# Performance work log

Hardware: AMD Instinct MI355X
Metric: run time of the kernel (lower is better)

The kernel has to match this reference:

```python
import jax, jax.numpy as jnp
import numpy as np

B, S, D = 4, 2048, 1024
H, HD = 16, 64
FF = 4096
EPS = 1e-5
NEG = -1000000.0


def setup_inputs() -> dict:
    key = jax.random.key(0)
    ks = jax.random.split(key, 12)
    sc = lambda n: 1.0 / np.sqrt(n)
    return {
        "x": jax.random.normal(ks[0], (B, S, D), jnp.float32),
        "valid_lens": jax.random.randint(ks[1], (B,), 1, S, jnp.int32),
        "Wq": jax.random.normal(ks[2], (D, H * HD), jnp.float32) * sc(D),
        "Wk": jax.random.normal(ks[3], (D, H * HD), jnp.float32) * sc(D),
        "Wv": jax.random.normal(ks[4], (D, H * HD), jnp.float32) * sc(D),
        "Wo": jax.random.normal(ks[5], (H * HD, D), jnp.float32) * sc(H * HD),
        "W1": jax.random.normal(ks[6], (D, FF), jnp.float32) * sc(D),
        "b1": jnp.zeros((FF,), jnp.float32),
        "W2": jax.random.normal(ks[7], (FF, D), jnp.float32) * sc(FF),
        "b2": jnp.zeros((D,), jnp.float32),
        "g1": jnp.ones((D,), jnp.float32),
        "beta1": jnp.zeros((D,), jnp.float32),
        "g2": jnp.ones((D,), jnp.float32),
        "beta2": jnp.zeros((D,), jnp.float32),
    }


def _layernorm(x, g, b):
    mu = jnp.mean(x, axis=-1, keepdims=True)
    var = jnp.var(x, axis=-1, keepdims=True)
    return (x - mu) * jax.lax.rsqrt(var + EPS) * g + b


def _encoder_block(x, valid_lens, Wq, Wk, Wv, Wo, W1, b1, W2, b2, g1, beta1, g2, beta2):
    # multi-head attention (vectorized over heads; masked softmax as in original)
    q = (x @ Wq).reshape(B, S, H, HD)
    k = (x @ Wk).reshape(B, S, H, HD)
    v = (x @ Wv).reshape(B, S, H, HD)
    scores = jnp.einsum("bqhd,bkhd->bhqk", q, k) / np.sqrt(HD)
    # mask: key positions >= valid_len[b] set to -1e6 (matches python-loop masking)
    col = jnp.arange(S)[None, None, None, :]           # [1,1,1,S]
    mask = col < valid_lens[:, None, None, None]       # [B,1,1,S]
    scores = jnp.where(mask, scores, NEG)
    w = jax.nn.softmax(scores, axis=-1)
    attn = jnp.einsum("bhqk,bkhd->bqhd", w, v).reshape(B, S, H * HD)
    attn_out = attn @ Wo
    res1 = _layernorm(attn_out + x, g1, beta1)
    ff = jax.nn.relu(res1 @ W1 + b1) @ W2 + b2
    return _layernorm(ff + res1, g2, beta2)


def reference(x, valid_lens, Wq, Wk, Wv, Wo, W1, b1, W2, b2, g1, beta1, g2, beta2):
    return _encoder_block(x, valid_lens, Wq, Wk, Wv, Wo, W1, b1, W2, b2, g1, beta1, g2, beta2)
```

## Files before the change

### kernel.cpp

```cpp
#include <hip/hip_runtime.h>
#include <hip/hip_bf16.h>
#include <stdint.h>

#define BB 4
#define SS 2048
#define DD 1024
#define HH 16
#define HD 64
#define FF 4096
#define MM (BB * SS)
#define BH (BB * HH)

typedef __bf16 bf16x8 __attribute__((ext_vector_type(8)));
typedef float f32x4 __attribute__((ext_vector_type(4)));

static __device__ __forceinline__ unsigned short f2bf(float f) {
  union { float f; unsigned u; } v; v.f = f;
  unsigned r = v.u + 0x7fffu + ((v.u >> 16) & 1u);
  return (unsigned short)(r >> 16);
}

static __device__ __forceinline__ unsigned packbf2(float a, float b) {
  __hip_bfloat162 h = __float22bfloat162_rn(float2{a, b});
  union { __hip_bfloat162 h; unsigned u; } cv; cv.h = h; return cv.u;
}

#define GLD_LDS16(SRC, DST)                                          \
  __builtin_amdgcn_global_load_lds(                                  \
      (const __attribute__((address_space(1))) void*)(SRC),          \
      (__attribute__((address_space(3))) void*)(DST), 16, 0, 0)

__global__ __launch_bounds__(256) void cast_bf16_k(const float* __restrict__ in,
                                                   unsigned short* __restrict__ out) {
  size_t i = ((size_t)blockIdx.x * 256 + threadIdx.x) * 4;
  float4 v = *(const float4*)(in + i);
  ushort4 u;
  u.x = f2bf(v.x); u.y = f2bf(v.y); u.z = f2bf(v.z); u.w = f2bf(v.w);
  *(ushort4*)(out + i) = u;
}

__global__ __launch_bounds__(256) void transpose_cast_k(const float* __restrict__ in,
                                                        unsigned short* __restrict__ out,
                                                        int K, int N) {
  __shared__ float tile[32][33];
  int n0 = blockIdx.x * 32, k0 = blockIdx.y * 32;
  int tx = threadIdx.x, ty = threadIdx.y;
#pragma unroll
  for (int i = 0; i < 32; i += 8)
    tile[ty + i][tx] = in[(size_t)(k0 + ty + i) * N + n0 + tx];
  __syncthreads();
#pragma unroll
  for (int i = 0; i < 32; i += 8)
    out[(size_t)(n0 + ty + i) * K + k0 + tx] = f2bf(tile[tx][ty + i]);
}

template <int EPI, int BN>
__global__ __launch_bounds__(512, 2) void gemm256(const unsigned short* __restrict__ A,
                                                  const unsigned short* __restrict__ BT,
                                                  const float* __restrict__ bias,
                                                  void* __restrict__ Cout,
                                                  int N, int K) {
  constexpr int BM = 256;
  constexpr int WN = BN / 4;
  constexpr int NR = WN / 16;
  constexpr int BCH = BN * 64 / 8 / 512;
  __shared__ __align__(16) unsigned short Al[2][BM * 64];
  __shared__ __align__(16) unsigned short Bl[2][BN * 64];
  const int t = threadIdx.x;
  const int w = t >> 6, l = t & 63, lr = l & 15, lg = l >> 4;
  const int wr = w >> 2, wc = w & 3;
  const int gx = gridDim.x;
  int lin = blockIdx.y * gx + blockIdx.x;
  const int nb = gx * gridDim.y;
  lin = (lin & 7) * (nb >> 3) + (lin >> 3);
  const int brow = (lin / gx) * BM, bcol = (lin % gx) * BN;
  f32x4 acc[8][NR] = {};

  auto stage = [&](int buf, int kt) {
#pragma unroll
    for (int i = 0; i < 4; ++i) {
      int c = i * 512 + t;
      int row = c >> 3;
      int js = (c & 7) ^ (row & 7);
      GLD_LDS16(A + (size_t)(brow + row) * K + kt * 64 + js * 8,
                &Al[buf][(i * 512 + w * 64) * 8]);
    }
#pragma unroll
    for (int i = 0; i < BCH; ++i) {
      int c = i * 512 + t;
      int row = c >> 3;
      int js = (c & 7) ^ (row & 7);
      GLD_LDS16(BT + (size_t)(bcol + row) * K + kt * 64 + js * 8,
                &Bl[buf][(i * 512 + w * 64) * 8]);
    }
  };

  const int nk = K >> 6;
  stage(0, 0);
  for (int kt = 0; kt < nk; ++kt) {
    const int cur = kt & 1;
    __syncthreads();
    if (kt + 1 < nk) stage(cur ^ 1, kt + 1);
#pragma unroll
    for (int kk = 0; kk < 2; ++kk) {
      bf16x8 af[8], bfr[NR];
#pragma unroll
      for (int m = 0; m < 8; ++m) {
        int row = wr * 128 + m * 16 + lr;
        af[m] = *(const bf16x8*)&Al[cur][row * 64 + (((kk * 4 + lg) ^ (row & 7)) << 3)];
      }
#pragma unroll
      for (int n = 0; n < NR; ++n) {
        int row = wc * WN + n * 16 + lr;
        bfr[n] = *(const bf16x8*)&Bl[cur][row * 64 + (((kk * 4 + lg) ^ (row & 7)) << 3)];
      }
      __builtin_amdgcn_s_setprio(1);
#pragma unroll
      for (int m = 0; m < 8; ++m)
#pragma unroll
        for (int n = 0; n < NR; ++n)
          acc[m][n] = __builtin_amdgcn_mfma_f32_16x16x32_bf16(af[m], bfr[n], acc[m][n], 0, 0, 0);
      __builtin_amdgcn_s_setprio(0);
    }
  }

#pragma unroll
  for (int m = 0; m < 8; ++m) {
#pragma unroll
    for (int n = 0; n < NR; ++n) {
      int col = bcol + wc * WN + n * 16 + lr;
      float bv = 0.f;
      if (EPI == 3 || EPI == 4) bv = bias[col];
#pragma unroll
      for (int i = 0; i < 4; ++i) {
        int row = brow + wr * 128 + m * 16 + lg * 4 + i;
        float v = acc[m][n][i];
        if (EPI == 0) {
          ((float*)Cout)[(size_t)row * N + col] = v;
        } else if (EPI == 3) {
          v += bv; v = v > 0.f ? v : 0.f;
          ((unsigned short*)Cout)[(size_t)row * N + col] = f2bf(v);
        } else if (EPI == 4) {
          v += bv;
          ((float*)Cout)[(size_t)row * N + col] = v;
        } else if (EPI == 5) {
          int b = row >> 11, s = row & 2047;
          int which = col >> 10, cin = col & 1023;
          int h = cin >> 6, hd = cin & 63;
          unsigned short* qb = (unsigned short*)Cout;
          if (which == 0) {
            qb[(((size_t)(b * HH + h)) * SS + s) * HD + hd] = f2bf(v * 0.125f);
          } else if (which == 1) {
            (qb + (size_t)MM * DD)[(((size_t)(b * HH + h)) * SS + s) * HD + hd] = f2bf(v);
          } else {
            (qb + 2 * (size_t)MM * DD)[(((size_t)(b * HH + h)) * HD + hd) * SS + s] = f2bf(v);
          }
        }
      }
    }
  }
}

__global__ __launch_bounds__(256, 4) void attn_kernel(const unsigned short* __restrict__ Q,
                                                      const unsigned short* __restrict__ Kg,
                                                      const unsigned short* __restrict__ VT,
                                                      const int* __restrict__ vlens,
                                                      unsigned short* __restrict__ O) {
  __shared__ __align__(16) unsigned short Kt[64 * 64];
  __shared__ __align__(16) unsigned short Vt[64 * 64];
  const int t = threadIdx.x;
  const int w = t >> 6, l = t & 63, lr = l & 15, lg = l >> 4;
  const int gid = blockIdx.x;
  const int bh = gid & 63, qb = gid >> 6;
  const int b = bh >> 4, h = bh & 15;
  const int q0 = qb << 6;
  const int vl = vlens[b];
  const size_t base = (size_t)bh * SS * HD;

  bf16x8 qf[2];
  {
    const int qrow = q0 + w * 16 + lr;
    qf[0] = *(const bf16x8*)(Q + base + (size_t)qrow * HD + lg * 8);
    qf[1] = *(const bf16x8*)(Q + base + (size_t)qrow * HD + 32 + lg * 8);
  }
  f32x4 o[4] = {};
  float m_r = -3.0e38f, l_r = 0.f;

  const int nkv = (vl + 63) >> 6;
  for (int kbi = 0; kbi < nkv; ++kbi) {
    const int kb = kbi << 6;
    __syncthreads();
#pragma unroll
    for (int is = 0; is < 2; ++is) {
      int c = is * 256 + t;
      int row = c >> 3;
      int js = (c & 7) ^ (row & 7);
      GLD_LDS16(Kg + base + (size_t)(kb + row) * HD + js * 8,
                &Kt[(is * 256 + w * 64) * 8]);
      GLD_LDS16(VT + base + (size_t)row * SS + kb + js * 8,
                &Vt[(is * 256 + w * 64) * 8]);
    }
    __syncthreads();

    f32x4 s[4] = {};
    __builtin_amdgcn_s_setprio(1);
#pragma unroll
    for (int kk = 0; kk < 2; ++kk)
#pragma unroll
      for (int n = 0; n < 4; ++n) {
        int row = n * 16 + lr;
        bf16x8 kf = *(const bf16x8*)&Kt[row * 64 + (((kk * 4 + lg) ^ (row & 7)) << 3)];
        s[n] = __builtin_amdgcn_mfma_f32_16x16x32_bf16(kf, qf[kk], s[n], 0, 0, 0);
      }
    __builtin_amdgcn_s_setprio(0);

    float sv[16];
    const int kbase = kb + lg * 4;
#pragma unroll
    for (int n = 0; n < 4; ++n)
#pragma unroll
      for (int i = 0; i < 4; ++i) {
        float v = s[n][i];
        if (kbase + n * 16 + i >= vl) v = -1.0e30f;
        sv[n * 4 + i] = v;
      }
    float tm[16];
#pragma unroll
    for (int j = 0; j < 16; ++j) tm[j] = sv[j];
#pragma unroll
    for (int st = 8; st >= 1; st >>= 1)
#pragma unroll
      for (int j = 0; j < 8; ++j)
        if (j < st) tm[j] = fmaxf(tm[j], tm[j + st]);
    float rm = tm[0];
    rm = fmaxf(rm, __shfl_xor(rm, 16));
    rm = fmaxf(rm, __shfl_xor(rm, 32));

    if (__any(rm > m_r + 8.f)) {
      float mnew = fmaxf(m_r, rm);
      float alpha = __expf(m_r - mnew);
      m_r = mnew;
      l_r *= alpha;
      float af[4];
#pragma unroll
      for (int i = 0; i < 4; ++i) af[i] = __shfl(alpha, lg * 4 + i);
#pragma unroll
      for (int n = 0; n < 4; ++n)
#pragma unroll
        for (int i = 0; i < 4; ++i) o[n][i] *= af[i];
    }

    float p[16];
#pragma unroll
    for (int j = 0; j < 16; ++j) p[j] = __expf(sv[j] - m_r);
    float ts[16];
#pragma unroll
    for (int j = 0; j < 16; ++j) ts[j] = p[j];
#pragma unroll
    for (int st = 8; st >= 1; st >>= 1)
#pragma unroll
      for (int j = 0; j < 8; ++j)
        if (j < st) ts[j] += ts[j + st];
    float rs = ts[0];
    rs += __shfl_xor(rs, 16);
    rs += __shfl_xor(rs, 32);
    l_r += rs;

    unsigned pd[4][2];
#pragma unroll
    for (int n = 0; n < 4; ++n) {
      pd[n][0] = packbf2(p[n * 4 + 0], p[n * 4 + 1]);
      pd[n][1] = packbf2(p[n * 4 + 2], p[n * 4 + 3]);
    }

#pragma unroll
    for (int kk = 0; kk < 2; ++kk) {
      unsigned pa[4];
#pragma unroll
      for (int jj = 0; jj < 4; ++jj) {
        int src = lr + 16 * (2 * (lg & 1) + (jj >> 1));
        unsigned rlo = __shfl(pd[2 * kk + 0][jj & 1], src);
        unsigned rhi = __shfl(pd[2 * kk + 1][jj & 1], src);
        pa[jj] = (lg & 2) ? rhi : rlo;
      }
      union { unsigned u[4]; bf16x8 v; } pb;
      pb.u[0] = pa[0]; pb.u[1] = pa[1]; pb.u[2] = pa[2]; pb.u[3] = pa[3];
      __builtin_amdgcn_s_setprio(1);
#pragma unroll
      for (int nd = 0; nd < 4; ++nd) {
        int row = nd * 16 + lr;
        bf16x8 vf = *(const bf16x8*)&Vt[row * 64 + (((kk * 4 + lg) ^ (row & 7)) << 3)];
        o[nd] = __builtin_amdgcn_mfma_f32_16x16x32_bf16(pb.v, vf, o[nd], 0, 0, 0);
      }
      __builtin_amdgcn_s_setprio(0);
    }
  }

  float linv[4];
#pragma unroll
  for (int i = 0; i < 4; ++i) linv[i] = 1.f / __shfl(l_r, lg * 4 + i);
#pragma unroll
  for (int nd = 0; nd < 4; ++nd)
#pragma unroll
    for (int i = 0; i < 4; ++i) {
      int qrow = q0 + w * 16 + lg * 4 + i;
      O[((size_t)b * SS + qrow) * DD + h * HD + nd * 16 + lr] = f2bf(o[nd][i] * linv[i]);
    }
}

__global__ __launch_bounds__(256) void ln_kernel(const float* __restrict__ a,
                                                 const float* __restrict__ bsrc,
                                                 const float* __restrict__ g,
                                                 const float* __restrict__ be,
                                                 float* __restrict__ outf,
                                                 unsigned short* __restrict__ outb) {
  const int row = blockIdx.x;
  const int t = threadIdx.x;
  const float4 av = ((const float4*)(a + (size_t)row * DD))[t];
  const float4 bv = ((const float4*)(bsrc + (size_t)row * DD))[t];
  float4 s;
  s.x = av.x + bv.x; s.y = av.y + bv.y; s.z = av.z + bv.z; s.w = av.w + bv.w;
  float sum = s.x + s.y + s.z + s.w;
  float sq = s.x * s.x + s.y * s.y + s.z * s.z + s.w * s.w;
#pragma unroll
  for (int mm = 1; mm < 64; mm <<= 1) {
    sum += __shfl_xor(sum, mm);
    sq += __shfl_xor(sq, mm);
  }
  __shared__ float red[8];
  const int w = t >> 6, l = t & 63;
  if (l == 0) { red[w] = sum; red[4 + w] = sq; }
  __syncthreads();
  sum = red[0] + red[1] + red[2] + red[3];
  sq = red[4] + red[5] + red[6] + red[7];
  const float mu = sum * (1.f / (float)DD);
  const float var = sq * (1.f / (float)DD) - mu * mu;
  const float rs = rsqrtf(var + 1e-5f);
  const float4 gv = ((const float4*)g)[t];
  const float4 bev = ((const float4*)be)[t];
  float4 y;
  y.x = (s.x - mu) * rs * gv.x + bev.x;
  y.y = (s.y - mu) * rs * gv.y + bev.y;
  y.z = (s.z - mu) * rs * gv.z + bev.z;
  y.w = (s.w - mu) * rs * gv.w + bev.w;
  if (outf) ((float4*)(outf + (size_t)row * DD))[t] = y;
  if (outb) {
    ushort4 u;
    u.x = f2bf(y.x); u.y = f2bf(y.y); u.z = f2bf(y.z); u.w = f2bf(y.w);
    ((ushort4*)(outb + (size_t)row * DD))[t] = u;
  }
}

extern "C" void kernel_launch(void* const* d_in, const int* in_sizes, int n_in,
                              void* d_out, int out_size, void* d_ws, size_t ws_size,
                              hipStream_t stream) {
  (void)in_sizes; (void)n_in; (void)out_size; (void)ws_size;
  const float* x = (const float*)d_in[0];
  const int* vlen = (const int*)d_in[1];
  const float* Wq = (const float*)d_in[2];
  const float* Wk = (const float*)d_in[3];
  const float* Wv = (const float*)d_in[4];
  const float* Wo = (const float*)d_in[5];
  const float* W1 = (const float*)d_in[6];
  const float* b1 = (const float*)d_in[7];
  const float* W2 = (const float*)d_in[8];
  const float* b2 = (const float*)d_in[9];
  const float* g1 = (const float*)d_in[10];
  const float* be1 = (const float*)d_in[11];
  const float* g2 = (const float*)d_in[12];
  const float* be2 = (const float*)d_in[13];
  float* out = (float*)d_out;

  char* ws = (char*)d_ws;
  size_t off = 0;
  auto alloc = [&](size_t bytes) {
    char* p = ws + off;
    off += (bytes + 255) & ~(size_t)255;
    return p;
  };
  unsigned short* xb = (unsigned short*)alloc((size_t)MM * DD * 2);
  unsigned short* WqT = (unsigned short*)alloc((size_t)DD * DD * 2);
  unsigned short* WkT = (unsigned short*)alloc((size_t)DD * DD * 2);
  unsigned short* WvT = (unsigned short*)alloc((size_t)DD * DD * 2);
  unsigned short* WoT = (unsigned short*)alloc((size_t)DD * DD * 2);
  unsigned short* W1T = (unsigned short*)alloc((size_t)FF * DD * 2);
  unsigned short* W2T = (unsigned short*)alloc((size_t)DD * FF * 2);
  unsigned short* Qb = (unsigned short*)alloc((size_t)MM * DD * 2);
  unsigned short* Kbb = (unsigned short*)alloc((size_t)MM * DD * 2);
  unsigned short* VTb = (unsigned short*)alloc((size_t)MM * DD * 2);
  unsigned short* attnb = (unsigned short*)alloc((size_t)MM * DD * 2);
  float* proj = (float*)alloc((size_t)MM * DD * 4);
  float* res1f = (float*)alloc((size_t)MM * DD * 4);
  unsigned short* res1b = (unsigned short*)alloc((size_t)MM * DD * 2);
  unsigned short* ff1 = Qb;
  float* ff2 = proj;
  (void)Kbb; (void)VTb;

  cast_bf16_k<<<MM * DD / 1024, 256, 0, stream>>>(x, xb);
  transpose_cast_k<<<dim3(32, 32), dim3(32, 8), 0, stream>>>(Wq, WqT, DD, DD);
  transpose_cast_k<<<dim3(32, 32), dim3(32, 8), 0, stream>>>(Wk, WkT, DD, DD);
  transpose_cast_k<<<dim3(32, 32), dim3(32, 8), 0, stream>>>(Wv, WvT, DD, DD);
  transpose_cast_k<<<dim3(32, 32), dim3(32, 8), 0, stream>>>(Wo, WoT, DD, DD);
  transpose_cast_k<<<dim3(128, 32), dim3(32, 8), 0, stream>>>(W1, W1T, DD, FF);
  transpose_cast_k<<<dim3(32, 128), dim3(32, 8), 0, stream>>>(W2, W2T, FF, DD);

  gemm256<5, 128><<<dim3(24, 32), 512, 0, stream>>>(xb, WqT, nullptr, Qb, 3072, DD);

  attn_kernel<<<dim3(2048), 256, 0, stream>>>(Qb, Kbb, VTb, vlen, attnb);

  gemm256<0, 128><<<dim3(8, 32), 512, 0, stream>>>(attnb, WoT, nullptr, proj, DD, DD);
  ln_kernel<<<MM, 256, 0, stream>>>(proj, x, g1, be1, res1f, res1b);
  gemm256<3, 256><<<dim3(16, 32), 512, 0, stream>>>(res1b, W1T, b1, ff1, FF, DD);
  gemm256<4, 128><<<dim3(8, 32), 512, 0, stream>>>(ff1, W2T, b2, ff2, DD, FF);
  ln_kernel<<<MM, 256, 0, stream>>>(ff2, res1f, g2, be2, out, nullptr);
}
```

Baseline: 465.3 us.

## Split GEMM k-step into four phases interleaving LDS reads, prefetch and MFMA

Replaces the double-buffered GEMM main loop with an eight-phase-style schedule. Each k-tile runs as four sub-phases, and each sub-phase issues LDS fragment reads and a slice of the next tile's global-to-LDS prefetch, then a barrier and a block of MFMAs. Explicit waitcnt, sched_barrier and s_barrier calls pin the interleaving. The FF1 GEMM drops its BN=256 tile and uses BN=128 with twice the grid. The extra barriers per k-tile may add sync overhead, and the smaller FF1 tile lowers data reuse.

```diff
diff --git a/kernel.cpp b/kernel.cpp
--- a/kernel.cpp
+++ b/kernel.cpp
@@ -54,16 +54,13 @@
     out[(size_t)(n0 + ty + i) * K + k0 + tx] = f2bf(tile[tx][ty + i]);
 }
 
-template <int EPI, int BN>
-__global__ __launch_bounds__(512, 2) void gemm256(const unsigned short* __restrict__ A,
-                                                  const unsigned short* __restrict__ BT,
-                                                  const float* __restrict__ bias,
-                                                  void* __restrict__ Cout,
-                                                  int N, int K) {
-  constexpr int BM = 256;
-  constexpr int WN = BN / 4;
-  constexpr int NR = WN / 16;
-  constexpr int BCH = BN * 64 / 8 / 512;
+template <int EPI>
+__global__ __launch_bounds__(512, 2) void gemm8p(const unsigned short* __restrict__ A,
+                                                 const unsigned short* __restrict__ BT,
+                                                 const float* __restrict__ bias,
+                                                 void* __restrict__ Cout,
+                                                 int N, int K) {
+  constexpr int BM = 256, BN = 128;
   __shared__ __align__(16) unsigned short Al[2][BM * 64];
   __shared__ __align__(16) unsigned short Bl[2][BN * 64];
   const int t = threadIdx.x;
@@ -74,19 +71,11 @@
   const int nb = gx * gridDim.y;
   lin = (lin & 7) * (nb >> 3) + (lin >> 3);
   const int brow = (lin / gx) * BM, bcol = (lin % gx) * BN;
-  f32x4 acc[8][NR] = {};
-
-  auto stage = [&](int buf, int kt) {
-#pragma unroll
-    for (int i = 0; i < 4; ++i) {
-      int c = i * 512 + t;
-      int row = c >> 3;
-      int js = (c & 7) ^ (row & 7);
-      GLD_LDS16(A + (size_t)(brow + row) * K + kt * 64 + js * 8,
-                &Al[buf][(i * 512 + w * 64) * 8]);
-    }
-#pragma unroll
-    for (int i = 0; i < BCH; ++i) {
+  f32x4 acc[8][2] = {};
+
+  auto stageB = [&](int buf, int kt) {
+#pragma unroll
+    for (int i = 0; i < 2; ++i) {
       int c = i * 512 + t;
       int row = c >> 3;
       int js = (c & 7) ^ (row & 7);
@@ -94,41 +83,99 @@
                 &Bl[buf][(i * 512 + w * 64) * 8]);
     }
   };
+  auto stageA = [&](int buf, int kt, int half) {
+#pragma unroll
+    for (int i = 0; i < 2; ++i) {
+      int c = half * 1024 + i * 512 + t;
+      int row = c >> 3;
+      int js = (c & 7) ^ (row & 7);
+      GLD_LDS16(A + (size_t)(brow + row) * K + kt * 64 + js * 8,
+                &Al[buf][(half * 1024 + i * 512 + w * 64) * 8]);
+    }
+  };
+  auto ldA = [&](bf16x8* af, int buf, int mh, int kk) {
+#pragma unroll
+    for (int m = 0; m < 4; ++m) {
+      int row = wr * 128 + (mh * 4 + m) * 16 + lr;
+      af[m] = *(const bf16x8*)&Al[buf][row * 64 + (((kk * 4 + lg) ^ (row & 7)) << 3)];
+    }
+  };
+  auto ldB = [&](bf16x8* bf, int buf, int kk) {
+#pragma unroll
+    for (int n = 0; n < 2; ++n) {
+      int row = wc * 32 + n * 16 + lr;
+      bf[n] = *(const bf16x8*)&Bl[buf][row * 64 + (((kk * 4 + lg) ^ (row & 7)) << 3)];
+    }
+  };
 
   const int nk = K >> 6;
-  stage(0, 0);
+  stageB(0, 0); stageA(0, 0, 0); stageA(0, 0, 1);
   for (int kt = 0; kt < nk; ++kt) {
-    const int cur = kt & 1;
-    __syncthreads();
-    if (kt + 1 < nk) stage(cur ^ 1, kt + 1);
-#pragma unroll
-    for (int kk = 0; kk < 2; ++kk) {
-      bf16x8 af[8], bfr[NR];
-#pragma unroll
-      for (int m = 0; m < 8; ++m) {
-        int row = wr * 128 + m * 16 + lr;
-        af[m] = *(const bf16x8*)&Al[cur][row * 64 + (((kk * 4 + lg) ^ (row & 7)) << 3)];
-      }
-#pragma unroll
-      for (int n = 0; n < NR; ++n) {
-        int row = wc * WN + n * 16 + lr;
-        bfr[n] = *(const bf16x8*)&Bl[cur][row * 64 + (((kk * 4 + lg) ^ (row & 7)) << 3)];
-      }
-      __builtin_amdgcn_s_setprio(1);
-#pragma unroll
-      for (int m = 0; m < 8; ++m)
-#pragma unroll
-        for (int n = 0; n < NR; ++n)
-          acc[m][n] = __builtin_amdgcn_mfma_f32_16x16x32_bf16(af[m], bfr[n], acc[m][n], 0, 0, 0);
-      __builtin_amdgcn_s_setprio(0);
-    }
+    const int p = kt & 1;
+    const bool pre = (kt + 1 < nk);
+    asm volatile("s_waitcnt vmcnt(0)" ::: "memory");
+    __builtin_amdgcn_sched_barrier(0);
+    __builtin_amdgcn_s_barrier();
+    __builtin_amdgcn_sched_barrier(0);
+
+    bf16x8 af[4], bf0[2], bf1[2];
+    ldA(af, p, 0, 0); ldB(bf0, p, 0);
+    if (pre) stageB(p ^ 1, kt + 1);
+    __builtin_amdgcn_s_barrier();
+    asm volatile("s_waitcnt lgkmcnt(0)" ::: "memory");
+    __builtin_amdgcn_sched_barrier(0);
+    __builtin_amdgcn_s_setprio(1);
+#pragma unroll
+    for (int m = 0; m < 4; ++m)
+#pragma unroll
+      for (int n = 0; n < 2; ++n)
+        acc[m][n] = __builtin_amdgcn_mfma_f32_16x16x32_bf16(af[m], bf0[n], acc[m][n], 0, 0, 0);
+    __builtin_amdgcn_s_setprio(0);
+
+    ldA(af, p, 1, 0);
+    if (pre) stageA(p ^ 1, kt + 1, 0);
+    __builtin_amdgcn_s_barrier();
+    asm volatile("s_waitcnt lgkmcnt(0)" ::: "memory");
+    __builtin_amdgcn_sched_barrier(0);
+    __builtin_amdgcn_s_setprio(1);
+#pragma unroll
+    for (int m = 0; m < 4; ++m)
+#pragma unroll
+      for (int n = 0; n < 2; ++n)
+        acc[4 + m][n] = __builtin_amdgcn_mfma_f32_16x16x32_bf16(af[m], bf0[n], acc[4 + m][n], 0, 0, 0);
+    __builtin_amdgcn_s_setprio(0);
+
+    ldA(af, p, 0, 1); ldB(bf1, p, 1);
+    if (pre) stageA(p ^ 1, kt + 1, 1);
+    __builtin_amdgcn_s_barrier();
+    asm volatile("s_waitcnt lgkmcnt(0)" ::: "memory");
+    __builtin_amdgcn_sched_barrier(0);
+    __builtin_amdgcn_s_setprio(1);
+#pragma unroll
+    for (int m = 0; m < 4; ++m)
+#pragma unroll
+      for (int n = 0; n < 2; ++n)
+        acc[m][n] = __builtin_amdgcn_mfma_f32_16x16x32_bf16(af[m], bf1[n], acc[m][n], 0, 0, 0);
+    __builtin_amdgcn_s_setprio(0);
+
+    ldA(af, p, 1, 1);
+    __builtin_amdgcn_s_barrier();
+    asm volatile("s_waitcnt lgkmcnt(0)" ::: "memory");
+    __builtin_amdgcn_sched_barrier(0);
+    __builtin_amdgcn_s_setprio(1);
+#pragma unroll
+    for (int m = 0; m < 4; ++m)
+#pragma unroll
+      for (int n = 0; n < 2; ++n)
+        acc[4 + m][n] = __builtin_amdgcn_mfma_f32_16x16x32_bf16(af[m], bf1[n], acc[4 + m][n], 0, 0, 0);
+    __builtin_amdgcn_s_setprio(0);
   }
 
 #pragma unroll
   for (int m = 0; m < 8; ++m) {
 #pragma unroll
-    for (int n = 0; n < NR; ++n) {
-      int col = bcol + wc * WN + n * 16 + lr;
+    for (int n = 0; n < 2; ++n) {
+      int col = bcol + wc * 32 + n * 16 + lr;
       float bv = 0.f;
       if (EPI == 3 || EPI == 4) bv = bias[col];
 #pragma unroll
@@ -404,13 +451,13 @@
   transpose_cast_k<<<dim3(128, 32), dim3(32, 8), 0, stream>>>(W1, W1T, DD, FF);
   transpose_cast_k<<<dim3(32, 128), dim3(32, 8), 0, stream>>>(W2, W2T, FF, DD);
 
-  gemm256<5, 128><<<dim3(24, 32), 512, 0, stream>>>(xb, WqT, nullptr, Qb, 3072, DD);
+  gemm8p<5><<<dim3(24, 32), 512, 0, stream>>>(xb, WqT, nullptr, Qb, 3072, DD);
 
   attn_kernel<<<dim3(2048), 256, 0, stream>>>(Qb, Kbb, VTb, vlen, attnb);
 
-  gemm256<0, 128><<<dim3(8, 32), 512, 0, stream>>>(attnb, WoT, nullptr, proj, DD, DD);
+  gemm8p<0><<<dim3(8, 32), 512, 0, stream>>>(attnb, WoT, nullptr, proj, DD, DD);
   ln_kernel<<<MM, 256, 0, stream>>>(proj, x, g1, be1, res1f, res1b);
-  gemm256<3, 256><<<dim3(16, 32), 512, 0, stream>>>(res1b, W1T, b1, ff1, FF, DD);
-  gemm256<4, 128><<<dim3(8, 32), 512, 0, stream>>>(ff1, W2T, b2, ff2, DD, FF);
+  gemm8p<3><<<dim3(32, 32), 512, 0, stream>>>(res1b, W1T, b1, ff1, FF, DD);
+  gemm8p<4><<<dim3(8, 32), 512, 0, stream>>>(ff1, W2T, b2, ff2, DD, FF);
   ln_kernel<<<MM, 256, 0, stream>>>(ff2, res1f, g2, be2, out, nullptr);
 }
```

After: 492.9 us. +5.9%, slower.
